# Performance work log

Hardware: AMD Instinct MI355X
Metric: run time of the kernel (lower is better)

## Reference

```python
import jax, jax.numpy as jnp
import numpy as np

EPS = 1e-20
STRIDE, PADDING, DILATION = 1, 2, 1


def setup_inputs() -> dict:
    key = jax.random.key(0)
    ks = jax.random.split(key, 8)
    B, C, O, H, W, K = 8, 32, 32, 256, 256, 5
    return {
        "d": jax.random.uniform(ks[0], (B, C, H, W), jnp.float32) + 0.1,   # positive depth
        "cd": jax.random.uniform(ks[1], (B, C, H, W), jnp.float32),        # depth confidence in [0,1)
        "gx": jax.random.normal(ks[2], (B, C, H, W), jnp.float32),         # x-gradient
        "cgx": jax.random.uniform(ks[3], (B, C, H, W), jnp.float32),       # gradient confidence
        "w_prop": jax.random.normal(ks[4], (1, C, 1, 1), jnp.float32) * 0.1,
        "spatial_weight": jax.random.normal(ks[5], (C, 1, K, K), jnp.float32) * 0.1,
        "channel_weight": jax.random.normal(ks[6], (O, C, 1, 1), jnp.float32) * 0.1,
        "bias": jax.random.normal(ks[7], (1, O, 1, 1), jnp.float32) * 0.01,
    }


def _conv(x, w, groups, stride=1, padding=0, dilation=1):
    return jax.lax.conv_general_dilated(
        x, w, (stride, stride), ((padding, padding), (padding, padding)),
        rhs_dilation=(dilation, dilation),
        dimension_numbers=("NCHW", "OIHW", "NCHW"),
        feature_group_count=groups)


def reference(d, cd, gx, cgx, w_prop, spatial_weight, channel_weight, bias):
    in_channels = d.shape[1]
    # EnforcePos reparameterization: effective weights = softplus(raw)
    wp = jax.nn.softplus(w_prop)
    sw = jax.nn.softplus(spatial_weight)
    cw = jax.nn.softplus(channel_weight)

    pad_w = lambda x, lr: jnp.pad(x, ((0, 0), (0, 0), (0, 0), lr))
    d_left = pad_w(d[..., :-1], (0, 1))
    cd_left = pad_w(cd[..., :-1], (0, 1))
    d_right = pad_w(d[..., 1:], (1, 0))
    cd_right = pad_w(cd[..., 1:], (1, 0))

    cgx_from_ds = cd_left * cd_right
    height = (cd_left * d_left + cd_right * d_right) / (cd_left + cd_right + EPS)
    gx_from_ds = (d_right - d_left) / 2 / (height + EPS)

    gx_prop = (wp * cgx * gx + cgx_from_ds * gx_from_ds) / (wp * cgx + cgx_from_ds + EPS)
    cgx_prop = (wp * cgx + cgx_from_ds) / (wp + 1)

    # depthwise spatial conv (groups = in_channels), then 1x1 channel conv
    nom = _conv(cgx_prop * gx_prop, sw, in_channels, STRIDE, PADDING, DILATION)
    denom = _conv(cgx_prop, sw, in_channels, STRIDE, PADDING, DILATION)
    gx_s = nom / (denom + EPS)
    cgx_s = denom / jnp.sum(sw)

    nom = _conv(cgx_s * gx_s, cw, 1)
    denom = _conv(cgx_s, cw, 1)
    gx_out = nom / (denom + EPS) + bias
    cgx_out = denom / jnp.sum(cw)
    return (gx_out * STRIDE, cgx_out / (STRIDE * STRIDE))
```

## Files before the change

### kernel.cpp

```cpp
#include <hip/hip_runtime.h>
#include <math.h>

constexpr int IMG_H = 256;
constexpr int IMG_W = 256;
constexpr int NB = 8;
constexpr int NC = 32;
constexpr int NO = 32;
constexpr int PLANE = IMG_H * IMG_W;
constexpr int HALF = NB * NC * PLANE;

constexpr int WTW = 16;
constexpr int WTH = 4;
constexpr int RR = WTH + 4;
constexpr int RC = 24;
constexpr int RSB = RC * 8;
constexpr int BUFB = RR * RSB;
constexpr int WLDS = 2 * BUFB;
constexpr int NWAVE = 4;
constexpr int NT = NWAVE * 64;
constexpr int NBLK = (IMG_W / WTW) * (IMG_H / WTH) * NB / NWAVE;

#define EPSV 1e-20f

typedef float f4 __attribute__((ext_vector_type(4)));
typedef float f2 __attribute__((ext_vector_type(2)));

__device__ __forceinline__ float rcpf_(float x) { return __builtin_amdgcn_rcpf(x); }
__device__ __forceinline__ float softplusf_(float x) {
  return fmaxf(x, 0.0f) + log1pf(expf(-fabsf(x)));
}

__global__ void weights_kernel(const float* __restrict__ wp_raw,
                               const float* __restrict__ sw_raw,
                               const float* __restrict__ cw_raw,
                               float* __restrict__ ws) {
  __shared__ float red[256];
  const int t = threadIdx.x;
  if (t < 32) ws[t] = softplusf_(wp_raw[t]);
  float ssum = 0.f;
  for (int i = t; i < NC * 25; i += 256) {
    float v = softplusf_(sw_raw[i]);
    ws[32 + i] = v;
    ssum += v;
  }
  float csum = 0.f;
  for (int i = t; i < NO * NC; i += 256) {
    float v = softplusf_(cw_raw[i]);
    int o = i >> 5, c = i & 31;
    ws[832 + c * NO + o] = v;
    csum += v;
  }
  red[t] = ssum; __syncthreads();
  for (int off = 128; off; off >>= 1) { if (t < off) red[t] += red[t + off]; __syncthreads(); }
  const float S_sw = red[0];
  __syncthreads();
  red[t] = csum; __syncthreads();
  for (int off = 128; off; off >>= 1) { if (t < off) red[t] += red[t + off]; __syncthreads(); }
  if (t == 0) { ws[1856] = S_sw; ws[1857] = red[0]; }
}

__device__ __forceinline__ void pointwise_pv(
    float dv, float cdv, float gxv, float cgv, int gw,
    float wpc, float inv_wp1, float& Pv, float& Vv) {
  float dl  = (gw == IMG_W - 1) ? 0.f : dv;
  float cdl = (gw == IMG_W - 1) ? 0.f : cdv;
  float dr  = (gw == 0) ? 0.f : dv;
  float cdr = (gw == 0) ? 0.f : cdv;
  float cfd = cdl * cdr;
  float height = (cdl * dl + cdr * dr) * rcpf_(cdl + cdr + EPSV);
  float gfd = (dr - dl) * 0.5f * rcpf_(height + EPSV);
  float den = fmaf(wpc, cgv, cfd);
  float num = fmaf(wpc * cgv, gxv, cfd * gfd);
  float gprop = num * rcpf_(den + EPSV);
  float cprop = den * inv_wp1;
  Pv = cprop;
  Vv = cprop * gprop;
}

__global__ __launch_bounds__(NT, 4) void fused_kernel(
    const float* __restrict__ dp, const float* __restrict__ cdp,
    const float* __restrict__ gxp, const float* __restrict__ cgxp,
    const float* __restrict__ ws, const float* __restrict__ bias,
    float* __restrict__ out) {
  __shared__ __align__(16) char shb[NWAVE * WLDS];

  const int t = threadIdx.x;
  const int wid = t >> 6;
  const int lane = t & 63;
  char* wbase = shb + wid * WLDS;

  const int wg = blockIdx.x;
  const int virt = (wg & 7) * (NBLK / 8) + (wg >> 3);
  const int b = virt >> 8;
  const int rem = virt & 255;
  const int ty = rem >> 2;
  const int qx = rem & 3;
  const int tx = qx * 4 + wid;
  const int w0 = tx * WTW, h0 = ty * WTH;

  const float Ssw = ws[1856], Scw = ws[1857];
  const float epsS = EPSV * Ssw;
  const float oscale = rcpf_(Ssw) * rcpf_(Scw);

  const bool sact = lane < 48;
  const int Rr = min(lane, 47) / 6;
  const int qq = min(lane, 47) - 6 * Rr;
  const int gh = h0 + Rr - 2;
  const int ghc = min(max(gh, 0), IMG_H - 1);
  const int gc0 = w0 - 4 + 4 * qq;
  const int gc0c = min(max(gc0, 0), IMG_W - 4);
  const int goff = ghc * IMG_W + gc0c;
  const bool rowv = (unsigned)gh < (unsigned)IMG_H;
  float msk[4];
  #pragma unroll
  for (int j = 0; j < 4; ++j)
    msk[j] = (rowv & ((unsigned)(gc0 + j) < (unsigned)IMG_W)) ? 1.f : 0.f;
  const int wb = Rr * RSB + qq * 32;

  const int x = lane & 15, y = lane >> 4;
  const int cvb = y * RSB + (x + 2) * 8;
  const int pixoff = (h0 + y) * IMG_W + (w0 + x);
  const int planebase = b * NC * PLANE;

  float accN[32], accD[32];
  #pragma unroll
  for (int o = 0; o < 32; ++o) { accN[o] = 0.f; accD[o] = 0.f; }

  f4 rd, rc, rg, rx;
  if (sact) {
    rd = *(const f4*)(dp + planebase + goff);
    rc = *(const f4*)(cdp + planebase + goff);
    rg = *(const f4*)(gxp + planebase + goff);
    rx = *(const f4*)(cgxp + planebase + goff);
  }

  #pragma unroll 1
  for (int c = 0; c < NC; ++c) {
    char* buf = wbase + (c & 1) * BUFB;
    const float wpc = ws[c];
    const float inv_wp1 = rcpf_(wpc + 1.0f);

    if (sact) {
      float P[4], V[4];
      #pragma unroll
      for (int j = 0; j < 4; ++j)
        pointwise_pv(rd[j], rc[j] * msk[j], rg[j], rx[j] * msk[j], gc0 + j,
                     wpc, inv_wp1, P[j], V[j]);
      f4 wv1; wv1[0] = P[0]; wv1[1] = V[0]; wv1[2] = P[1]; wv1[3] = V[1];
      f4 wv2; wv2[0] = P[2]; wv2[1] = V[2]; wv2[2] = P[3]; wv2[3] = V[3];
      *(f4*)(buf + wb) = wv1;
      *(f4*)(buf + wb + 16) = wv2;
    }

    if ((c + 1 < NC) & sact) {
      const int pb = planebase + (c + 1) * PLANE + goff;
      rd = *(const f4*)(dp + pb);
      rc = *(const f4*)(cdp + pb);
      rg = *(const f4*)(gxp + pb);
      rx = *(const f4*)(cgxp + pb);
    }

    asm volatile("s_waitcnt lgkmcnt(0)" ::: "memory");

    const char* bp = buf + cvb;
    const float* swc = ws + 32 + c * 25;
    float Dc = 0.f, Nc = 0.f;
    #pragma unroll
    for (int kr = 0; kr < 5; ++kr) {
      #pragma unroll
      for (int kc = 0; kc < 5; ++kc) {
        const f2 pv = *(const f2*)(bp + kr * RSB + kc * 8);
        const float wv = swc[kr * 5 + kc];
        Dc = fmaf(wv, pv[0], Dc);
        Nc = fmaf(wv, pv[1], Nc);
      }
    }

    const float* cwc = ws + 832 + c * NO;
    #pragma unroll
    for (int o = 0; o < 32; ++o) {
      accD[o] = fmaf(cwc[o], Dc, accD[o]);
      accN[o] = fmaf(cwc[o], Nc, accN[o]);
    }
  }

  const int ob = b * NO * PLANE + pixoff;
  #pragma unroll
  for (int o = 0; o < 32; ++o) {
    const float g = fmaf(accN[o], rcpf_(accD[o] + epsS), bias[o]);
    const float cg = accD[o] * oscale;
    out[ob + o * PLANE] = g;
    out[HALF + ob + o * PLANE] = cg;
  }
}

extern "C" void kernel_launch(void* const* d_in, const int* in_sizes, int n_in,
                              void* d_out, int out_size, void* d_ws, size_t ws_size,
                              hipStream_t stream) {
  const float* dp   = (const float*)d_in[0];
  const float* cdp  = (const float*)d_in[1];
  const float* gxp  = (const float*)d_in[2];
  const float* cgxp = (const float*)d_in[3];
  const float* wp   = (const float*)d_in[4];
  const float* sw   = (const float*)d_in[5];
  const float* cw   = (const float*)d_in[6];
  const float* bias = (const float*)d_in[7];
  float* out = (float*)d_out;
  float* ws  = (float*)d_ws;

  weights_kernel<<<1, 256, 0, stream>>>(wp, sw, cw, ws);
  fused_kernel<<<NBLK, NT, 0, stream>>>(dp, cdp, gxp, cgxp, ws, bias, out);
}
```

Before: 405.7 us.

## Process two channels per loop iteration with deeper prefetch and LDS buffers

Unrolls the channel loop by two, so each iteration computes pointwise terms, the depthwise 5x5 conv and the 1x1 accumulation for a pair of channels. Global loads for the next two channels are issued together, and the per-wave LDS buffer grows from two to four slots. The goal is more memory-level parallelism and fewer loop and wait overheads per channel. In exchange it uses more VGPRs for the extra prefetch registers and doubles LDS per block, which may lower occupancy under the 4-blocks launch bound.

After: 413.5 us. About the same (+1.9%).

```diff
diff --git a/kernel.cpp b/kernel.cpp
--- a/kernel.cpp
+++ b/kernel.cpp
@@ -15,7 +15,7 @@
 constexpr int RC = 24;
 constexpr int RSB = RC * 8;
 constexpr int BUFB = RR * RSB;
-constexpr int WLDS = 2 * BUFB;
+constexpr int WLDS = 4 * BUFB;
 constexpr int NWAVE = 4;
 constexpr int NT = NWAVE * 64;
 constexpr int NBLK = (IMG_W / WTW) * (IMG_H / WTH) * NB / NWAVE;
@@ -126,61 +126,83 @@
   #pragma unroll
   for (int o = 0; o < 32; ++o) { accN[o] = 0.f; accD[o] = 0.f; }
 
-  f4 rd, rc, rg, rx;
+  f4 dA, cA, gA, xA, dB, cB, gB, xB;
   if (sact) {
-    rd = *(const f4*)(dp + planebase + goff);
-    rc = *(const f4*)(cdp + planebase + goff);
-    rg = *(const f4*)(gxp + planebase + goff);
-    rx = *(const f4*)(cgxp + planebase + goff);
+    const int p0 = planebase + goff;
+    dA = *(const f4*)(dp + p0);  cA = *(const f4*)(cdp + p0);
+    gA = *(const f4*)(gxp + p0); xA = *(const f4*)(cgxp + p0);
+    const int p1 = p0 + PLANE;
+    dB = *(const f4*)(dp + p1);  cB = *(const f4*)(cdp + p1);
+    gB = *(const f4*)(gxp + p1); xB = *(const f4*)(cgxp + p1);
   }
 
   #pragma unroll 1
-  for (int c = 0; c < NC; ++c) {
-    char* buf = wbase + (c & 1) * BUFB;
-    const float wpc = ws[c];
-    const float inv_wp1 = rcpf_(wpc + 1.0f);
+  for (int g = 0; g < NC; g += 2) {
+    const int q = (g >> 1) & 1;
+    char* bufA = wbase + (2 * q) * BUFB;
+    char* bufB = wbase + (2 * q + 1) * BUFB;
+
+    const float wpA = ws[g], wpB = ws[g + 1];
+    const float invA = rcpf_(wpA + 1.0f), invB = rcpf_(wpB + 1.0f);
 
     if (sact) {
       float P[4], V[4];
       #pragma unroll
       for (int j = 0; j < 4; ++j)
-        pointwise_pv(rd[j], rc[j] * msk[j], rg[j], rx[j] * msk[j], gc0 + j,
-                     wpc, inv_wp1, P[j], V[j]);
-      f4 wv1; wv1[0] = P[0]; wv1[1] = V[0]; wv1[2] = P[1]; wv1[3] = V[1];
-      f4 wv2; wv2[0] = P[2]; wv2[1] = V[2]; wv2[2] = P[3]; wv2[3] = V[3];
-      *(f4*)(buf + wb) = wv1;
-      *(f4*)(buf + wb + 16) = wv2;
-    }
-
-    if ((c + 1 < NC) & sact) {
-      const int pb = planebase + (c + 1) * PLANE + goff;
-      rd = *(const f4*)(dp + pb);
-      rc = *(const f4*)(cdp + pb);
-      rg = *(const f4*)(gxp + pb);
-      rx = *(const f4*)(cgxp + pb);
+        pointwise_pv(dA[j], cA[j] * msk[j], gA[j], xA[j] * msk[j], gc0 + j,
+                     wpA, invA, P[j], V[j]);
+      f4 w1; w1[0] = P[0]; w1[1] = V[0]; w1[2] = P[1]; w1[3] = V[1];
+      f4 w2; w2[0] = P[2]; w2[1] = V[2]; w2[2] = P[3]; w2[3] = V[3];
+      *(f4*)(bufA + wb) = w1;
+      *(f4*)(bufA + wb + 16) = w2;
+      #pragma unroll
+      for (int j = 0; j < 4; ++j)
+        pointwise_pv(dB[j], cB[j] * msk[j], gB[j], xB[j] * msk[j], gc0 + j,
+                     wpB, invB, P[j], V[j]);
+      f4 w3; w3[0] = P[0]; w3[1] = V[0]; w3[2] = P[1]; w3[3] = V[1];
+      f4 w4; w4[0] = P[2]; w4[1] = V[2]; w4[2] = P[3]; w4[3] = V[3];
+      *(f4*)(bufB + wb) = w3;
+      *(f4*)(bufB + wb + 16) = w4;
+    }
+
+    if ((g + 2 < NC) & sact) {
+      const int pA = planebase + (g + 2) * PLANE + goff;
+      dA = *(const f4*)(dp + pA);  cA = *(const f4*)(cdp + pA);
+      gA = *(const f4*)(gxp + pA); xA = *(const f4*)(cgxp + pA);
+      const int pB = pA + PLANE;
+      dB = *(const f4*)(dp + pB);  cB = *(const f4*)(cdp + pB);
+      gB = *(const f4*)(gxp + pB); xB = *(const f4*)(cgxp + pB);
     }
 
     asm volatile("s_waitcnt lgkmcnt(0)" ::: "memory");
 
-    const char* bp = buf + cvb;
-    const float* swc = ws + 32 + c * 25;
-    float Dc = 0.f, Nc = 0.f;
+    const char* bpA = bufA + cvb;
+    const char* bpB = bufB + cvb;
+    const float* swA = ws + 32 + g * 25;
+    const float* swB = swA + 25;
+    float DA = 0.f, NA = 0.f, DB = 0.f, NBv = 0.f;
     #pragma unroll
     for (int kr = 0; kr < 5; ++kr) {
       #pragma unroll
       for (int kc = 0; kc < 5; ++kc) {
-        const f2 pv = *(const f2*)(bp + kr * RSB + kc * 8);
-        const float wv = swc[kr * 5 + kc];
-        Dc = fmaf(wv, pv[0], Dc);
-        Nc = fmaf(wv, pv[1], Nc);
+        const int off = kr * RSB + kc * 8;
+        const f2 pvA = *(const f2*)(bpA + off);
+        const f2 pvB = *(const f2*)(bpB + off);
+        const float wA = swA[kr * 5 + kc];
+        const float wB = swB[kr * 5 + kc];
+        DA  = fmaf(wA, pvA[0], DA);
+        NA  = fmaf(wA, pvA[1], NA);
+        DB  = fmaf(wB, pvB[0], DB);
+        NBv = fmaf(wB, pvB[1], NBv);
       }
     }
 
-    const float* cwc = ws + 832 + c * NO;
+    const float* cwA = ws + 832 + g * NO;
+    const float* cwB = cwA + NO;
     #pragma unroll
     for (int o = 0; o < 32; ++o) {
-      accD[o] = fmaf(cwc[o], Dc, accD[o]);
-      accN[o] = fmaf(cwc[o], Nc, accN[o]);
+      accD[o] = fmaf(cwB[o], DB, fmaf(cwA[o], DA, accD[o]));
+      accN[o] = fmaf(cwB[o], NBv, fmaf(cwA[o], NA, accN[o]));
     }
   }
 
```
